# Kernel tuning notes

Hardware: AMD Instinct MI355X
Metric: run time of the kernel (lower is better)

## Reference

```python
import jax, jax.numpy as jnp
import numpy as np


def setup_inputs() -> dict:
    key = jax.random.key(0)
    k1, k2 = jax.random.split(key)
    B, N, M = 8, 8192, 8192
    pred = jax.random.normal(k1, (B, N, 3), dtype=jnp.float32)
    target = jax.random.normal(k2, (B, M, 3), dtype=jnp.float32)
    return {"pred": pred, "target": target}


def reference(pred, target):
    # pairwise squared distances: (B, N, M)
    pred_sq = jnp.sum(pred ** 2, axis=2, keepdims=True)            # (B, N, 1)
    target_sq = jnp.sum(target ** 2, axis=2, keepdims=True)        # (B, M, 1)
    dist = pred_sq + jnp.swapaxes(target_sq, 1, 2) \
           - 2.0 * jnp.einsum('bnd,bmd->bnm', pred, target)
    dist = jnp.maximum(dist, 0.0)
    cd_p2t = jnp.mean(jnp.min(dist, axis=2))   # pred -> target
    cd_t2p = jnp.mean(jnp.min(dist, axis=1))   # target -> pred (bidirectional=True)
    return cd_p2t + cd_t2p
```

## Files before the change

kernel.cpp:

```cpp
#include <hip/hip_runtime.h>
#include <math.h>

#define THREADS  256
#define NPTS     8192
#define BATCH    8
#define ENTRIES  (2 * BATCH * NPTS)
#define ENC_U4   (2 * BATCH * NPTS / 1024 * 2048)
#define ENC_BYTES ((size_t)ENC_U4 * 16)
#define MINS_BYTES ((size_t)2 * ENTRIES * 4)
#define WS1_BYTES (ENC_BYTES + MINS_BYTES)
#define WS_BYTES  ((size_t)ENTRIES * 4)

typedef __attribute__((ext_vector_type(8)))  short bf16x8;
typedef __attribute__((ext_vector_type(16))) float f32x16;

union FragCast { uint4 u; bf16x8 v; };

__device__ __forceinline__ unsigned short f2bf(float f) {
    unsigned u = __float_as_uint(f);
    unsigned r = (u + 0x7FFFu + ((u >> 16) & 1u)) >> 16;
    return (unsigned short)r;
}
__device__ __forceinline__ float bf2f(unsigned short h) {
    return __uint_as_float(((unsigned)h) << 16);
}
#define PK(a, b) (((unsigned)(a)) | (((unsigned)(b)) << 16))
#define BF_ONE 0x3F80u

__device__ __forceinline__ void async_copy16(void* lds_dst, const void* g_src) {
    __builtin_amdgcn_global_load_lds(
        (const __attribute__((address_space(1))) unsigned*)g_src,
        (__attribute__((address_space(3))) unsigned*)lds_dst,
        16, 0, 0);
}

__device__ __forceinline__ void encode_db_point(float x, float y, float z,
                                                uint4& h0, uint4& h1) {
    const float sq = fmaf(x, x, fmaf(y, y, z * z));
    const unsigned short xh = f2bf(x), yh = f2bf(y), zh = f2bf(z);
    const unsigned short xl = f2bf(x - bf2f(xh));
    const unsigned short yl = f2bf(y - bf2f(yh));
    const unsigned short zl = f2bf(z - bf2f(zh));
    const unsigned short sh = f2bf(sq);
    const unsigned short sl = f2bf(sq - bf2f(sh));
    h0 = make_uint4(PK(xh, yh), PK(zh, xl), PK(yl, zl), PK(xh, yh));
    h1 = make_uint4(PK(zh, xl), PK(yl, zl), PK(sh, sl), PK(BF_ONE, BF_ONE));
}

__global__ __launch_bounds__(THREADS)
void chamfer_encode_kernel(const float* __restrict__ pred,
                           const float* __restrict__ target,
                           uint4* __restrict__ enc)
{
    const int t   = blockIdx.x * THREADS + threadIdx.x;
    const int arr = t >> 16;
    const int rem = t & 0xFFFF;
    const int b   = rem >> 13;
    const int p   = rem & (NPTS - 1);
    const float* src = (arr ? target : pred) + ((size_t)b * NPTS + p) * 3;
    uint4 h0, h1;
    encode_db_point(src[0], src[1], src[2], h0, h1);
    const int chunk = p >> 10, pl = p & 1023;
    const int j = pl >> 5, c = pl & 31;
    uint4* base = enc + ((size_t)((arr * BATCH + b) * 8 + chunk)) * 2048;
    base[j * 64 + c]      = h0;
    base[j * 64 + c + 32] = h1;
}

__global__ __launch_bounds__(THREADS, 4)
void chamfer_mfma3_kernel(const float* __restrict__ pred,
                          const float* __restrict__ target,
                          const uint4* __restrict__ enc,
                          float* __restrict__ mins)
{
    __shared__ uint4 lds[2048];

    const int bx  = blockIdx.x;
    const int ds  = bx & 1;
    const int qb  = (bx >> 1) & 31;
    const int b   = (bx >> 6) & 7;
    const int dir = bx >> 9;

    const float* qarr = dir ? target : pred;
    const int arr_db  = dir ^ 1;

    const int tid  = threadIdx.x;
    const int ln   = tid & 63;
    const int w    = tid >> 6;
    const int half = ln >> 5;

    bf16x8 bq0, bq1;
    const int qbase = qb * 256 + w * 64;
    #pragma unroll
    for (int nb = 0; nb < 2; ++nb) {
        const int qi = qbase + nb * 32 + (ln & 31);
        const float* qp = qarr + ((size_t)b * NPTS + qi) * 3;
        const float x = qp[0], y = qp[1], z = qp[2];
        const float sq = fmaf(x, x, fmaf(y, y, z * z));
        const float wx = -2.0f * x, wy = -2.0f * y, wz = -2.0f * z;
        const unsigned short wxh = f2bf(wx), wyh = f2bf(wy), wzh = f2bf(wz);
        const unsigned short wxl = f2bf(wx - bf2f(wxh));
        const unsigned short wyl = f2bf(wy - bf2f(wyh));
        const unsigned short wzl = f2bf(wz - bf2f(wzh));
        const unsigned short sh  = f2bf(sq);
        const unsigned short sl  = f2bf(sq - bf2f(sh));
        FragCast fc;
        if (half == 0) fc.u = make_uint4(PK(wxh, wyh), PK(wzh, wxh), PK(wyh, wzh), PK(wxl, wyl));
        else           fc.u = make_uint4(PK(wzl, wxl), PK(wyl, wzl), PK(BF_ONE, BF_ONE), PK(sh, sl));
        if (nb == 0) bq0 = fc.v; else bq1 = fc.v;
    }

    const f32x16 zacc = {};
    f32x16 m0, m1;
    #pragma unroll
    for (int i = 0; i < 16; ++i) { m0[i] = INFINITY; m1[i] = INFINITY; }

    for (int chunk = 0; chunk < 4; ++chunk) {
        const uint4* gch = enc + ((size_t)((arr_db * BATCH + b) * 8 + ds * 4 + chunk)) * 2048;
        #pragma unroll
        for (int k = 0; k < 8; ++k) {
            const int blk = w * 8 + k;
            async_copy16(&lds[blk * 64], gch + blk * 64 + ln);
        }
        __syncthreads();

        #pragma unroll 2
        for (int j = 0; j < 32; j += 2) {
            FragCast a0, a1;
            a0.u = lds[j * 64 + ln];
            a1.u = lds[(j + 1) * 64 + ln];
            const f32x16 c00 = __builtin_amdgcn_mfma_f32_32x32x16_bf16(a0.v, bq0, zacc, 0, 0, 0);
            const f32x16 c01 = __builtin_amdgcn_mfma_f32_32x32x16_bf16(a1.v, bq0, zacc, 0, 0, 0);
            #pragma unroll
            for (int i = 0; i < 16; ++i)
                m0[i] = fminf(fminf(m0[i], c00[i]), c01[i]);
            const f32x16 c10 = __builtin_amdgcn_mfma_f32_32x32x16_bf16(a0.v, bq1, zacc, 0, 0, 0);
            const f32x16 c11 = __builtin_amdgcn_mfma_f32_32x32x16_bf16(a1.v, bq1, zacc, 0, 0, 0);
            #pragma unroll
            for (int i = 0; i < 16; ++i)
                m1[i] = fminf(fminf(m1[i], c10[i]), c11[i]);
        }
        __syncthreads();
    }

    float r0, r1;
    {
        float a0 = fminf(fminf(m0[0], m0[1]), fminf(m0[2], m0[3]));
        float a1 = fminf(fminf(m0[4], m0[5]), fminf(m0[6], m0[7]));
        float a2 = fminf(fminf(m0[8], m0[9]), fminf(m0[10], m0[11]));
        float a3 = fminf(fminf(m0[12], m0[13]), fminf(m0[14], m0[15]));
        r0 = fminf(fminf(a0, a1), fminf(a2, a3));
        float b0 = fminf(fminf(m1[0], m1[1]), fminf(m1[2], m1[3]));
        float b1 = fminf(fminf(m1[4], m1[5]), fminf(m1[6], m1[7]));
        float b2 = fminf(fminf(m1[8], m1[9]), fminf(m1[10], m1[11]));
        float b3 = fminf(fminf(m1[12], m1[13]), fminf(m1[14], m1[15]));
        r1 = fminf(fminf(b0, b1), fminf(b2, b3));
    }
    r0 = fminf(r0, __shfl_xor(r0, 32, 64));
    r1 = fminf(r1, __shfl_xor(r1, 32, 64));
    if (ln < 32) {
        const int base = ds * ENTRIES + dir * (BATCH * NPTS) + b * NPTS + qbase;
        mins[base + ln]      = r0;
        mins[base + 32 + ln] = r1;
    }
}

__global__ __launch_bounds__(THREADS)
void chamfer_finish3_kernel(const float* __restrict__ mins,
                            float* __restrict__ out,
                            float inv_count)
{
    const int t = blockIdx.x * THREADS + threadIdx.x;
    const float4* p0 = (const float4*)mins;
    const float4* p1 = (const float4*)(mins + ENTRIES);
    float s = 0.0f;
    #pragma unroll
    for (int k = 0; k < 2; ++k) {
        const int i4 = t * 2 + k;
        const float4 a = p0[i4];
        const float4 c = p1[i4];
        s += fmaxf(fminf(a.x, c.x), 0.0f) + fmaxf(fminf(a.y, c.y), 0.0f)
           + fmaxf(fminf(a.z, c.z), 0.0f) + fmaxf(fminf(a.w, c.w), 0.0f);
    }
    float v = s;
    #pragma unroll
    for (int off = 32; off > 0; off >>= 1)
        v += __shfl_down(v, off, 64);
    __shared__ float wsum[THREADS / 64];
    if ((threadIdx.x & 63) == 0) wsum[threadIdx.x >> 6] = v;
    __syncthreads();
    if (threadIdx.x == 0)
        atomicAdd(out, (wsum[0] + wsum[1] + wsum[2] + wsum[3]) * inv_count);
}

__global__ __launch_bounds__(THREADS, 4)
void chamfer_mfma_kernel(const float* __restrict__ pred,
                         const float* __restrict__ target,
                         unsigned* __restrict__ wskeys)
{
    __shared__ short lds[32 * 64 * 8];
    const int bx  = blockIdx.x;
    const int ds  = bx & 3;
    const int qb  = (bx >> 2) & 15;
    const int b   = (bx >> 6) & 7;
    const int dir = bx >> 9;
    const float* qarr = dir ? target : pred;
    const float* darr = dir ? pred   : target;
    const int tid  = threadIdx.x;
    const int ln   = tid & 63;
    const int w    = tid >> 6;
    const int half = ln >> 5;

    bf16x8 bq[4];
    const int qbase = qb * 512 + w * 128;
    #pragma unroll
    for (int nb = 0; nb < 4; ++nb) {
        const int qi = qbase + nb * 32 + (ln & 31);
        const float* qp = qarr + ((size_t)b * NPTS + qi) * 3;
        const float x = qp[0], y = qp[1], z = qp[2];
        const float sq = fmaf(x, x, fmaf(y, y, z * z));
        const float wx = -2.0f * x, wy = -2.0f * y, wz = -2.0f * z;
        const unsigned short wxh = f2bf(wx), wyh = f2bf(wy), wzh = f2bf(wz);
        const unsigned short wxl = f2bf(wx - bf2f(wxh));
        const unsigned short wyl = f2bf(wy - bf2f(wyh));
        const unsigned short wzl = f2bf(wz - bf2f(wzh));
        const unsigned short sh  = f2bf(sq);
        const unsigned short sl  = f2bf(sq - bf2f(sh));
        FragCast fc;
        if (half == 0) fc.u = make_uint4(PK(wxh, wyh), PK(wzh, wxh), PK(wyh, wzh), PK(wxl, wyl));
        else           fc.u = make_uint4(PK(wzl, wxl), PK(wyl, wzl), PK(BF_ONE, BF_ONE), PK(sh, sl));
        bq[nb] = fc.v;
    }

    float mn[4] = {INFINITY, INFINITY, INFINITY, INFINITY};
    const int range0 = ds * 2048;
    for (int chunk = 0; chunk < 2; ++chunk) {
        #pragma unroll
        for (int it = 0; it < 4; ++it) {
            const int pl = it * THREADS + tid;
            const int p  = range0 + chunk * 1024 + pl;
            const float* tp = darr + ((size_t)b * NPTS + p) * 3;
            uint4 h0, h1;
            encode_db_point(tp[0], tp[1], tp[2], h0, h1);
            const int j = pl >> 5, c = pl & 31;
            *(uint4*)&lds[(j * 64 + c) * 8]      = h0;
            *(uint4*)&lds[(j * 64 + c + 32) * 8] = h1;
        }
        __syncthreads();
        #pragma unroll 4
        for (int j = 0; j < 32; ++j) {
            const bf16x8 a = *(const bf16x8*)&lds[(j * 64 + ln) * 8];
            f32x16 z = {};
            f32x16 c0 = __builtin_amdgcn_mfma_f32_32x32x16_bf16(a, bq[0], z, 0, 0, 0);
            f32x16 c1 = __builtin_amdgcn_mfma_f32_32x32x16_bf16(a, bq[1], z, 0, 0, 0);
            f32x16 c2 = __builtin_amdgcn_mfma_f32_32x32x16_bf16(a, bq[2], z, 0, 0, 0);
            f32x16 c3 = __builtin_amdgcn_mfma_f32_32x32x16_bf16(a, bq[3], z, 0, 0, 0);
            #pragma unroll
            for (int i = 0; i < 16; i += 2) {
                mn[0] = fminf(mn[0], fminf(c0[i], c0[i + 1]));
                mn[1] = fminf(mn[1], fminf(c1[i], c1[i + 1]));
                mn[2] = fminf(mn[2], fminf(c2[i], c2[i + 1]));
                mn[3] = fminf(mn[3], fminf(c3[i], c3[i + 1]));
            }
        }
        __syncthreads();
    }
    const int obase = dir * (BATCH * NPTS) + b * NPTS;
    #pragma unroll
    for (int nb = 0; nb < 4; ++nb) {
        const float o = __shfl_xor(mn[nb], 32, 64);
        const float m = fminf(mn[nb], o);
        if (ln < 32) {
            const unsigned u   = __float_as_uint(m);
            const unsigned key = (u >> 31) ? ~u : (u | 0x80000000u);
            atomicMin(&wskeys[obase + qbase + nb * 32 + ln], key);
        }
    }
}

__global__ __launch_bounds__(THREADS)
void chamfer_finish_kernel(const unsigned* __restrict__ ws,
                           float* __restrict__ out,
                           float inv_count)
{
    const int t = blockIdx.x * THREADS + threadIdx.x;
    const uint4 kk = ((const uint4*)ws)[t];
    float s = 0.0f;
    { const unsigned u = (kk.x >> 31) ? (kk.x ^ 0x80000000u) : ~kk.x; s += fmaxf(__uint_as_float(u), 0.0f); }
    { const unsigned u = (kk.y >> 31) ? (kk.y ^ 0x80000000u) : ~kk.y; s += fmaxf(__uint_as_float(u), 0.0f); }
    { const unsigned u = (kk.z >> 31) ? (kk.z ^ 0x80000000u) : ~kk.z; s += fmaxf(__uint_as_float(u), 0.0f); }
    { const unsigned u = (kk.w >> 31) ? (kk.w ^ 0x80000000u) : ~kk.w; s += fmaxf(__uint_as_float(u), 0.0f); }
    float v = s;
    #pragma unroll
    for (int off = 32; off > 0; off >>= 1)
        v += __shfl_down(v, off, 64);
    __shared__ float wsum[THREADS / 64];
    if ((threadIdx.x & 63) == 0) wsum[threadIdx.x >> 6] = v;
    __syncthreads();
    if (threadIdx.x == 0)
        atomicAdd(out, (wsum[0] + wsum[1] + wsum[2] + wsum[3]) * inv_count);
}

__global__ __launch_bounds__(THREADS, 2)
void chamfer_fallback_kernel(const float* __restrict__ pred,
                             const float* __restrict__ target,
                             float* __restrict__ out,
                             float inv_count)
{
    __shared__ float4 lds[2048];
    const float* q  = (blockIdx.y == 0) ? pred   : target;
    const float* db = (blockIdx.y == 0) ? target : pred;
    const int b = blockIdx.x / (NPTS / THREADS);
    const int n = (blockIdx.x % (NPTS / THREADS)) * THREADS + threadIdx.x;
    const float* qp = q + ((size_t)b * NPTS + n) * 3;
    const float px = qp[0], py = qp[1], pz = qp[2];
    const float npx = -2.0f * px, npy = -2.0f * py, npz = -2.0f * pz;
    const float P = px * px + py * py + pz * pz;
    const float* dbB = db + (size_t)b * NPTS * 3;
    float m0 = INFINITY;
    for (int c0 = 0; c0 < NPTS; c0 += 2048) {
        for (int k = 0; k < 2048 / THREADS; ++k) {
            const int j = k * THREADS + threadIdx.x;
            const float* tp = dbB + (size_t)(c0 + j) * 3;
            const float tx = tp[0], ty = tp[1], tz = tp[2];
            lds[j] = make_float4(tx, ty, tz, tx * tx + ty * ty + tz * tz);
        }
        __syncthreads();
        for (int j = 0; j < 2048; ++j) {
            const float4 T = lds[j];
            m0 = fminf(m0, fmaf(npx, T.x, fmaf(npy, T.y, fmaf(npz, T.z, T.w))));
        }
        __syncthreads();
    }
    float v = fmaxf(P + m0, 0.0f);
    #pragma unroll
    for (int off = 32; off > 0; off >>= 1)
        v += __shfl_down(v, off, 64);
    __shared__ float wsum[THREADS / 64];
    if ((threadIdx.x & 63) == 0) wsum[threadIdx.x >> 6] = v;
    __syncthreads();
    if (threadIdx.x == 0)
        atomicAdd(out, (wsum[0] + wsum[1] + wsum[2] + wsum[3]) * inv_count);
}

extern "C" void kernel_launch(void* const* d_in, const int* in_sizes, int n_in,
                              void* d_out, int out_size, void* d_ws, size_t ws_size,
                              hipStream_t stream) {
    const float* pred   = (const float*)d_in[0];
    const float* target = (const float*)d_in[1];
    float* out = (float*)d_out;
    const float inv_count = 1.0f / (float)(BATCH * NPTS);

    if (ws_size >= WS1_BYTES) {
        uint4* enc  = (uint4*)d_ws;
        float* mins = (float*)((char*)d_ws + ENC_BYTES);
        hipMemsetAsync(out, 0, out_size * sizeof(float), stream);
        chamfer_encode_kernel<<<(2 * BATCH * NPTS) / THREADS, THREADS, 0, stream>>>(pred, target, enc);
        chamfer_mfma3_kernel<<<1024, THREADS, 0, stream>>>(pred, target, enc, mins);
        chamfer_finish3_kernel<<<ENTRIES / (THREADS * 8), THREADS, 0, stream>>>(mins, out, inv_count);
    } else if (ws_size >= WS_BYTES) {
        hipMemsetAsync(out, 0, out_size * sizeof(float), stream);
        unsigned* ws = (unsigned*)d_ws;
        hipMemsetAsync(ws, 0xFF, WS_BYTES, stream);
        chamfer_mfma_kernel<<<1024, THREADS, 0, stream>>>(pred, target, ws);
        chamfer_finish_kernel<<<ENTRIES / (THREADS * 4), THREADS, 0, stream>>>(ws, out, inv_count);
    } else {
        hipMemsetAsync(out, 0, out_size * sizeof(float), stream);
        dim3 grid(BATCH * (NPTS / THREADS), 2);
        chamfer_fallback_kernel<<<grid, THREADS, 0, stream>>>(pred, target, out, inv_count);
    }
}
```

Before: 96.92 us.

## Split database into four planes, read fragments directly from global, fold memset into encode

The MFMA kernel now splits each query block's database sweep four ways instead of two, launching twice as many blocks, and the finish kernel reduces across four partial-min planes. The LDS staging with async copies and barriers is removed, so each wave loads its bf16 fragments straight from global memory (L2-resident encoded data). The output zeroing moves from a separate memset into the encode kernel. This aims to raise occupancy and drop sync and launch overhead, at the cost of duplicate global reads per wave and more partial-min traffic.

Result: slower. 375.5 us (+287.5%).

```diff
diff --git a/kernel.cpp b/kernel.cpp
--- a/kernel.cpp
+++ b/kernel.cpp
@@ -5,9 +5,10 @@
 #define NPTS     8192
 #define BATCH    8
 #define ENTRIES  (2 * BATCH * NPTS)
-#define ENC_U4   (2 * BATCH * NPTS / 1024 * 2048)
+#define ENC_U4   (2 * BATCH * 8 * 2048)
 #define ENC_BYTES ((size_t)ENC_U4 * 16)
-#define MINS_BYTES ((size_t)2 * ENTRIES * 4)
+#define NPLANES  4
+#define MINS_BYTES ((size_t)NPLANES * ENTRIES * 4)
 #define WS1_BYTES (ENC_BYTES + MINS_BYTES)
 #define WS_BYTES  ((size_t)ENTRIES * 4)
 
@@ -26,13 +27,6 @@
 }
 #define PK(a, b) (((unsigned)(a)) | (((unsigned)(b)) << 16))
 #define BF_ONE 0x3F80u
-
-__device__ __forceinline__ void async_copy16(void* lds_dst, const void* g_src) {
-    __builtin_amdgcn_global_load_lds(
-        (const __attribute__((address_space(1))) unsigned*)g_src,
-        (__attribute__((address_space(3))) unsigned*)lds_dst,
-        16, 0, 0);
-}
 
 __device__ __forceinline__ void encode_db_point(float x, float y, float z,
                                                 uint4& h0, uint4& h1) {
@@ -50,9 +44,11 @@
 __global__ __launch_bounds__(THREADS)
 void chamfer_encode_kernel(const float* __restrict__ pred,
                            const float* __restrict__ target,
-                           uint4* __restrict__ enc)
+                           uint4* __restrict__ enc,
+                           float* __restrict__ out)
 {
     const int t   = blockIdx.x * THREADS + threadIdx.x;
+    if (t == 0) out[0] = 0.0f;
     const int arr = t >> 16;
     const int rem = t & 0xFFFF;
     const int b   = rem >> 13;
@@ -60,26 +56,23 @@
     const float* src = (arr ? target : pred) + ((size_t)b * NPTS + p) * 3;
     uint4 h0, h1;
     encode_db_point(src[0], src[1], src[2], h0, h1);
-    const int chunk = p >> 10, pl = p & 1023;
-    const int j = pl >> 5, c = pl & 31;
-    uint4* base = enc + ((size_t)((arr * BATCH + b) * 8 + chunk)) * 2048;
-    base[j * 64 + c]      = h0;
-    base[j * 64 + c + 32] = h1;
-}
-
-__global__ __launch_bounds__(THREADS, 4)
-void chamfer_mfma3_kernel(const float* __restrict__ pred,
+    const int T = p >> 5, c = p & 31;
+    uint4* base = enc + (size_t)(arr * BATCH + b) * 16384;
+    base[T * 64 + c]      = h0;
+    base[T * 64 + c + 32] = h1;
+}
+
+__global__ __launch_bounds__(THREADS, 8)
+void chamfer_mfma4_kernel(const float* __restrict__ pred,
                           const float* __restrict__ target,
                           const uint4* __restrict__ enc,
                           float* __restrict__ mins)
 {
-    __shared__ uint4 lds[2048];
-
     const int bx  = blockIdx.x;
-    const int ds  = bx & 1;
-    const int qb  = (bx >> 1) & 31;
-    const int b   = (bx >> 6) & 7;
-    const int dir = bx >> 9;
+    const int ds  = bx & 3;
+    const int qb  = (bx >> 2) & 31;
+    const int b   = (bx >> 7) & 7;
+    const int dir = bx >> 10;
 
     const float* qarr = dir ? target : pred;
     const int arr_db  = dir ^ 1;
@@ -115,32 +108,23 @@
     #pragma unroll
     for (int i = 0; i < 16; ++i) { m0[i] = INFINITY; m1[i] = INFINITY; }
 
-    for (int chunk = 0; chunk < 4; ++chunk) {
-        const uint4* gch = enc + ((size_t)((arr_db * BATCH + b) * 8 + ds * 4 + chunk)) * 2048;
+    const uint4* gbase = enc + (size_t)(arr_db * BATCH + b) * 16384 + ds * 4096 + ln;
+
+    #pragma unroll 2
+    for (int jj = 0; jj < 64; jj += 2) {
+        FragCast a0, a1;
+        a0.u = gbase[jj * 64];
+        a1.u = gbase[jj * 64 + 64];
+        const f32x16 c00 = __builtin_amdgcn_mfma_f32_32x32x16_bf16(a0.v, bq0, zacc, 0, 0, 0);
+        const f32x16 c01 = __builtin_amdgcn_mfma_f32_32x32x16_bf16(a1.v, bq0, zacc, 0, 0, 0);
         #pragma unroll
-        for (int k = 0; k < 8; ++k) {
-            const int blk = w * 8 + k;
-            async_copy16(&lds[blk * 64], gch + blk * 64 + ln);
-        }
-        __syncthreads();
-
-        #pragma unroll 2
-        for (int j = 0; j < 32; j += 2) {
-            FragCast a0, a1;
-            a0.u = lds[j * 64 + ln];
-            a1.u = lds[(j + 1) * 64 + ln];
-            const f32x16 c00 = __builtin_amdgcn_mfma_f32_32x32x16_bf16(a0.v, bq0, zacc, 0, 0, 0);
-            const f32x16 c01 = __builtin_amdgcn_mfma_f32_32x32x16_bf16(a1.v, bq0, zacc, 0, 0, 0);
-            #pragma unroll
-            for (int i = 0; i < 16; ++i)
-                m0[i] = fminf(fminf(m0[i], c00[i]), c01[i]);
-            const f32x16 c10 = __builtin_amdgcn_mfma_f32_32x32x16_bf16(a0.v, bq1, zacc, 0, 0, 0);
-            const f32x16 c11 = __builtin_amdgcn_mfma_f32_32x32x16_bf16(a1.v, bq1, zacc, 0, 0, 0);
-            #pragma unroll
-            for (int i = 0; i < 16; ++i)
-                m1[i] = fminf(fminf(m1[i], c10[i]), c11[i]);
-        }
-        __syncthreads();
+        for (int i = 0; i < 16; ++i)
+            m0[i] = fminf(fminf(m0[i], c00[i]), c01[i]);
+        const f32x16 c10 = __builtin_amdgcn_mfma_f32_32x32x16_bf16(a0.v, bq1, zacc, 0, 0, 0);
+        const f32x16 c11 = __builtin_amdgcn_mfma_f32_32x32x16_bf16(a1.v, bq1, zacc, 0, 0, 0);
+        #pragma unroll
+        for (int i = 0; i < 16; ++i)
+            m1[i] = fminf(fminf(m1[i], c10[i]), c11[i]);
     }
 
     float r0, r1;
@@ -166,22 +150,20 @@
 }
 
 __global__ __launch_bounds__(THREADS)
-void chamfer_finish3_kernel(const float* __restrict__ mins,
+void chamfer_finish4_kernel(const float* __restrict__ mins,
                             float* __restrict__ out,
                             float inv_count)
 {
     const int t = blockIdx.x * THREADS + threadIdx.x;
     const float4* p0 = (const float4*)mins;
     const float4* p1 = (const float4*)(mins + ENTRIES);
-    float s = 0.0f;
-    #pragma unroll
-    for (int k = 0; k < 2; ++k) {
-        const int i4 = t * 2 + k;
-        const float4 a = p0[i4];
-        const float4 c = p1[i4];
-        s += fmaxf(fminf(a.x, c.x), 0.0f) + fmaxf(fminf(a.y, c.y), 0.0f)
-           + fmaxf(fminf(a.z, c.z), 0.0f) + fmaxf(fminf(a.w, c.w), 0.0f);
-    }
+    const float4* p2 = (const float4*)(mins + 2 * ENTRIES);
+    const float4* p3 = (const float4*)(mins + 3 * ENTRIES);
+    const float4 a = p0[t], c = p1[t], d = p2[t], e = p3[t];
+    float s = fmaxf(fminf(fminf(a.x, c.x), fminf(d.x, e.x)), 0.0f)
+            + fmaxf(fminf(fminf(a.y, c.y), fminf(d.y, e.y)), 0.0f)
+            + fmaxf(fminf(fminf(a.z, c.z), fminf(d.z, e.z)), 0.0f)
+            + fmaxf(fminf(fminf(a.w, c.w), fminf(d.w, e.w)), 0.0f);
     float v = s;
     #pragma unroll
     for (int off = 32; off > 0; off >>= 1)
@@ -354,10 +336,11 @@
     if (ws_size >= WS1_BYTES) {
         uint4* enc  = (uint4*)d_ws;
         float* mins = (float*)((char*)d_ws + ENC_BYTES);
-        hipMemsetAsync(out, 0, out_size * sizeof(float), stream);
-        chamfer_encode_kernel<<<(2 * BATCH * NPTS) / THREADS, THREADS, 0, stream>>>(pred, target, enc);
-        chamfer_mfma3_kernel<<<1024, THREADS, 0, stream>>>(pred, target, enc, mins);
-        chamfer_finish3_kernel<<<ENTRIES / (THREADS * 8), THREADS, 0, stream>>>(mins, out, inv_count);
+        chamfer_encode_kernel<<<(2 * BATCH * NPTS) / THREADS, THREADS, 0, stream>>>(
+            pred, target, enc, out);
+        chamfer_mfma4_kernel<<<2048, THREADS, 0, stream>>>(pred, target, enc, mins);
+        chamfer_finish4_kernel<<<ENTRIES / (THREADS * 4), THREADS, 0, stream>>>(
+            mins, out, inv_count);
     } else if (ws_size >= WS_BYTES) {
         hipMemsetAsync(out, 0, out_size * sizeof(float), stream);
         unsigned* ws = (unsigned*)d_ws;
```
